# Kernel optimization log

Hardware: AMD Instinct MI355X
Metric: run time of the kernel (lower is better)

## Reference

```python
import jax, jax.numpy as jnp
import numpy as np

EMB = 1024
HEADS = 16
HEAD_DIM = EMB // HEADS


def setup_inputs() -> dict:
    key = jax.random.key(0)
    ks = jax.random.split(key, 9)
    s = 1.0 / np.sqrt(EMB)  # torch Linear default init scale (uniform), use normal*s for simplicity of magnitude
    x = jax.random.normal(ks[0], (2, 2048, EMB), dtype=jnp.float32)
    wQ = jax.random.uniform(ks[1], (EMB, EMB), jnp.float32, -s, s)
    bQ = jax.random.uniform(ks[2], (EMB,), jnp.float32, -s, s)
    wK = jax.random.uniform(ks[3], (EMB, EMB), jnp.float32, -s, s)
    bK = jax.random.uniform(ks[4], (EMB,), jnp.float32, -s, s)
    wV = jax.random.uniform(ks[5], (EMB, EMB), jnp.float32, -s, s)
    bV = jax.random.uniform(ks[6], (EMB,), jnp.float32, -s, s)
    wO = jax.random.uniform(ks[7], (EMB, EMB), jnp.float32, -s, s)
    bO = jax.random.uniform(ks[8], (EMB,), jnp.float32, -s, s)
    return {"x": x, "wQ": wQ, "bQ": bQ, "wK": wK, "bK": bK, "wV": wV, "bV": bV, "wO": wO, "bO": bO}


def reference(x, wQ, bQ, wK, bK, wV, bV, wO, bO):
    B, S, E = x.shape
    H, Dh = HEADS, HEAD_DIM
    # manual LayerNorm-like scaling; torch.std uses unbiased (ddof=1)
    mu = jnp.mean(x, axis=-1, keepdims=True)
    sd = jnp.std(x, axis=-1, keepdims=True, ddof=1)
    xn = (x - mu) / (sd + 1e-6)
    # torch Linear: y = x @ W.T + b
    q = (xn @ wQ.T + bQ).reshape(B, S, H, Dh).transpose(0, 2, 1, 3)  # [B,H,S,Dh]
    k = (xn @ wK.T + bK).reshape(B, S, H, Dh).transpose(0, 2, 1, 3)
    v = (xn @ wV.T + bV).reshape(B, S, H, Dh).transpose(0, 2, 1, 3)
    scores = jnp.einsum('bhsd,bhtd->bhst', q, k) / np.sqrt(Dh).astype(np.float32)
    A = jax.nn.softmax(scores, axis=-1)
    Hout = jnp.einsum('bhst,bhtd->bhsd', A, v)  # [B,H,S,Dh]
    Hout = Hout.transpose(0, 2, 1, 3).reshape(B, S, E)
    return Hout @ wO.T + bO
```

## Files before the change

kernel.cpp:

```cpp
#include <hip/hip_runtime.h>
#include <cstdint>
#include <cstddef>

typedef __bf16 bf16x8 __attribute__((ext_vector_type(8)));
typedef float f32x4 __attribute__((ext_vector_type(4)));
typedef unsigned short us4 __attribute__((ext_vector_type(4)));
typedef unsigned short us8 __attribute__((ext_vector_type(8)));
typedef unsigned int ui4 __attribute__((ext_vector_type(4)));
typedef unsigned short u16;

#define QSCALE 0.18033688011112042f

#define MFMA16(a, b, c) __builtin_amdgcn_mfma_f32_16x16x32_bf16((a), (b), (c), 0, 0, 0)
#define GLOAD16(g, l)                                                        \
  __builtin_amdgcn_global_load_lds(                                          \
      (const __attribute__((address_space(1))) void*)(g),                    \
      (__attribute__((address_space(3))) void*)(l), 16, 0, 0)

__device__ __forceinline__ u16 f2bf(float x) {
  unsigned int u = __float_as_uint(x);
  unsigned int r = u + 0x7fffu + ((u >> 16) & 1u);
  return (u16)(r >> 16);
}

__global__ __launch_bounds__(256) void prep_kernel(
    const float* __restrict__ x, const float* __restrict__ wq,
    const float* __restrict__ wk, const float* __restrict__ wv,
    const float* __restrict__ wo, u16* __restrict__ xn,
    u16* __restrict__ wdst) {
  const int bid = blockIdx.x;
  const int t = threadIdx.x;
  if (bid < 4096) {
    const int row = bid;
    const float* xr = x + (size_t)row * 1024;
    float4 v = *(const float4*)(xr + t * 4);
    float s = v.x + v.y + v.z + v.w;
    float s2 = v.x * v.x + v.y * v.y + v.z * v.z + v.w * v.w;
#pragma unroll
    for (int o = 32; o >= 1; o >>= 1) {
      s += __shfl_xor(s, o);
      s2 += __shfl_xor(s2, o);
    }
    __shared__ float red[8];
    const int wv_ = t >> 6, ln = t & 63;
    if (ln == 0) {
      red[wv_] = s;
      red[4 + wv_] = s2;
    }
    __syncthreads();
    s = red[0] + red[1] + red[2] + red[3];
    s2 = red[4] + red[5] + red[6] + red[7];
    const float mu = s * (1.0f / 1024.0f);
    float var = (s2 - 1024.0f * mu * mu) * (1.0f / 1023.0f);
    var = fmaxf(var, 0.0f);
    const float inv = 1.0f / (sqrtf(var) + 1e-6f);
    us4 o;
    o.x = f2bf((v.x - mu) * inv);
    o.y = f2bf((v.y - mu) * inv);
    o.z = f2bf((v.z - mu) * inv);
    o.w = f2bf((v.w - mu) * inv);
    *(us4*)(xn + (size_t)row * 1024 + t * 4) = o;
  } else {
    const int wid = bid - 4096;
    const int mat = wid >> 9, xi = wid & 511;
    const float* src = (mat == 0) ? wq : (mat == 1) ? wk : (mat == 2) ? wv : wo;
    const float sc = (mat == 0) ? QSCALE : 1.0f;
    u16* d = wdst + ((size_t)mat << 20);
    const size_t i = ((size_t)xi * 256 + t) * 8;
    float4 a = *(const float4*)(src + i);
    float4 b = *(const float4*)(src + i + 4);
    us8 o;
    o[0] = f2bf(a.x * sc);
    o[1] = f2bf(a.y * sc);
    o[2] = f2bf(a.z * sc);
    o[3] = f2bf(a.w * sc);
    o[4] = f2bf(b.x * sc);
    o[5] = f2bf(b.y * sc);
    o[6] = f2bf(b.z * sc);
    o[7] = f2bf(b.w * sc);
    *(us8*)(d + i) = o;
  }
}

__device__ __forceinline__ void gemm128_core(const u16* __restrict__ A,
                                             const u16* __restrict__ W,
                                             int m0, int n0,
                                             u16 (*As)[128 * 32],
                                             u16 (*Bs)[128 * 32],
                                             f32x4 acc[4][4]) {
  const int tid = threadIdx.x;
  const int lane = tid & 63, wave = tid >> 6;
  const int wm = wave >> 1, wn = wave & 1;
  const int lr = lane & 15, lg = lane >> 4;

  auto stage = [&](int buf, int kt) {
#pragma unroll
    for (int i = 0; i < 2; i++) {
      const int idx = i * 256 + tid;
      const int row = idx >> 2, ch = idx & 3;
      const int sc = ch ^ ((row >> 1) & 3);
      GLOAD16(A + (size_t)(m0 + row) * 1024 + kt * 32 + sc * 8,
              &As[buf][idx * 8]);
      GLOAD16(W + (size_t)(n0 + row) * 1024 + kt * 32 + sc * 8,
              &Bs[buf][idx * 8]);
    }
  };

  stage(0, 0);
  const int cs = (lg ^ ((lr >> 1) & 3)) * 8;
  int cur = 0;
  for (int kt = 0; kt < 32; ++kt) {
    __syncthreads();
    if (kt + 1 < 32) stage(cur ^ 1, kt + 1);
    bf16x8 af[4], bfr[4];
#pragma unroll
    for (int m = 0; m < 4; m++)
      af[m] = *(const bf16x8*)&As[cur][(wm * 64 + m * 16 + lr) * 32 + cs];
#pragma unroll
    for (int n = 0; n < 4; n++)
      bfr[n] = *(const bf16x8*)&Bs[cur][(wn * 64 + n * 16 + lr) * 32 + cs];
#pragma unroll
    for (int m = 0; m < 4; m++)
#pragma unroll
      for (int n = 0; n < 4; n++)
        acc[m][n] = MFMA16(af[m], bfr[n], acc[m][n]);
    cur ^= 1;
  }
}

__global__ __launch_bounds__(256) void qkv_gemm(
    const u16* __restrict__ xn, const u16* __restrict__ Wall,
    const float* __restrict__ bQ, const float* __restrict__ bK,
    const float* __restrict__ bV, u16* __restrict__ Qb, u16* __restrict__ Kb,
    u16* __restrict__ VTb) {
  __shared__ u16 As[2][128 * 32];
  __shared__ u16 Bs[2][128 * 32];
  const int z = blockIdx.z;
  const u16* W = Wall + ((size_t)z << 20);
  const float* bias = (z == 0) ? bQ : (z == 1) ? bK : bV;
  const float bscale = (z == 0) ? QSCALE : 1.0f;
  const int m0 = blockIdx.x * 128, n0 = blockIdx.y * 128;
  f32x4 acc[4][4] = {};
  gemm128_core(xn, W, m0, n0, As, Bs, acc);

  const int lane = threadIdx.x & 63, wave = threadIdx.x >> 6;
  const int wm = wave >> 1, wn = wave & 1, lr = lane & 15, lg = lane >> 4;
  if (z == 2) {
#pragma unroll
    for (int n = 0; n < 4; n++) {
      const int col = n0 + wn * 64 + n * 16 + lr;
      const float bv = bias[col];
      const int hh = col >> 6, d = col & 63;
#pragma unroll
      for (int m = 0; m < 4; m++) {
        const int rb = m0 + wm * 64 + m * 16 + lg * 4;
#pragma unroll
        for (int j = 0; j < 4; j++) {
          const int row = rb + j;
          const int bb = row >> 11, s = row & 2047;
          VTb[(((size_t)(bb * 16 + hh) * 64 + d) << 11) + s] =
              f2bf(acc[m][n][j] + bv);
        }
      }
    }
  } else {
    u16* o = (z == 0) ? Qb : Kb;
#pragma unroll
    for (int n = 0; n < 4; n++) {
      const int col = n0 + wn * 64 + n * 16 + lr;
      const float bv = bias[col] * bscale;
#pragma unroll
      for (int m = 0; m < 4; m++) {
        const int rb = m0 + wm * 64 + m * 16 + lg * 4;
#pragma unroll
        for (int j = 0; j < 4; j++)
          o[(size_t)(rb + j) * 1024 + col] = f2bf(acc[m][n][j] + bv);
      }
    }
  }
}

__global__ __launch_bounds__(256) void o_gemm(const u16* __restrict__ A,
                                              const u16* __restrict__ W,
                                              const float* __restrict__ bias,
                                              float* __restrict__ out) {
  __shared__ u16 As[2][128 * 32];
  __shared__ u16 Bs[2][128 * 32];
  const int m0 = blockIdx.x * 128, n0 = blockIdx.y * 128;
  f32x4 acc[4][4] = {};
  gemm128_core(A, W, m0, n0, As, Bs, acc);
  const int lane = threadIdx.x & 63, wave = threadIdx.x >> 6;
  const int wm = wave >> 1, wn = wave & 1, lr = lane & 15, lg = lane >> 4;
#pragma unroll
  for (int n = 0; n < 4; n++) {
    const int col = n0 + wn * 64 + n * 16 + lr;
    const float bv = bias[col];
#pragma unroll
    for (int m = 0; m < 4; m++) {
      const int rb = m0 + wm * 64 + m * 16 + lg * 4;
#pragma unroll
      for (int j = 0; j < 4; j++)
        out[(size_t)(rb + j) * 1024 + col] = acc[m][n][j] + bv;
    }
  }
}

__global__ __launch_bounds__(256, 2) void attn_kernel(
    const u16* __restrict__ Qb, const u16* __restrict__ Kb,
    const u16* __restrict__ VTb, u16* __restrict__ Hb) {
  __shared__ u16 Ks[2][128 * 64];
  __shared__ u16 Vs[2][64 * 128];
  const int tid = threadIdx.x;
  const int wave = tid >> 6, lane = tid & 63;
  const int lr = lane & 15, lg = lane >> 4;
  const int qb = blockIdx.x, bh = blockIdx.y;
  const int b = bh >> 4, h = bh & 15;

  bf16x8 aq[2][2];
#pragma unroll
  for (int qg = 0; qg < 2; qg++) {
    const int qrow = b * 2048 + qb * 128 + wave * 32 + qg * 16 + lr;
    const u16* qsrc = Qb + (size_t)qrow * 1024 + h * 64 + lg * 8;
    aq[qg][0] = *(const bf16x8*)qsrc;
    aq[qg][1] = *(const bf16x8*)(qsrc + 32);
  }

  float l_run[2] = {0.0f, 0.0f};
  f32x4 oacc[2][4] = {};

  auto stage = [&](int buf, int kt) {
#pragma unroll
    for (int i = 0; i < 4; i++) {
      const int idx = i * 256 + tid;
      const int r = idx >> 3, c = idx & 7;
      GLOAD16(Kb + (size_t)(b * 2048 + kt * 128 + r) * 1024 + h * 64 +
                  (c ^ (r & 7)) * 8,
              &Ks[buf][idx * 8]);
    }
#pragma unroll
    for (int i = 0; i < 4; i++) {
      const int idx = i * 256 + tid;
      const int r = idx >> 4, c = idx & 15;
      GLOAD16(VTb + (size_t)(bh * 64 + r) * 2048 + kt * 128 +
                  (c ^ (r & 7)) * 8,
              &Vs[buf][idx * 8]);
    }
  };

  auto softpack = [&](f32x4 (&s)[8], float& lsum, ui4 (&pf)[4]) {
    float ls = 0.0f;
#pragma unroll
    for (int n = 0; n < 8; n++) {
#pragma unroll
      for (int j = 0; j < 4; j++) {
        s[n][j] = __builtin_amdgcn_exp2f(s[n][j]);
        ls += s[n][j];
      }
    }
    lsum += ls;
    unsigned int w[8][2];
#pragma unroll
    for (int n = 0; n < 8; n++) {
      asm("v_cvt_pk_bf16_f32 %0, %1, %2"
          : "=v"(w[n][0])
          : "v"(s[n][0]), "v"(s[n][1]));
      asm("v_cvt_pk_bf16_f32 %0, %1, %2"
          : "=v"(w[n][1])
          : "v"(s[n][2]), "v"(s[n][3]));
    }
#pragma unroll
    for (int ks = 0; ks < 4; ks++) {
      unsigned int pw[4];
#pragma unroll
      for (int rp = 0; rp < 2; rp++) {
        unsigned int a = w[2 * ks][rp], bb = w[2 * ks + 1][rp];
        asm("v_permlane32_swap_b32 %0, %1" : "+v"(a), "+v"(bb));
        asm("v_permlane16_swap_b32 %0, %1" : "+v"(a), "+v"(bb));
        pw[rp] = a;
        pw[2 + rp] = bb;
      }
      pf[ks] = (ui4){pw[0], pw[1], pw[2], pw[3]};
    }
  };

  stage(0, 0);
  int cur = 0;
  for (int kt = 0; kt < 16; ++kt) {
    __syncthreads();
    if (kt + 1 < 16) stage(cur ^ 1, kt + 1);

    f32x4 s0[8], s1[8];
#pragma unroll
    for (int n = 0; n < 8; n++) {
      s0[n] = (f32x4){0.f, 0.f, 0.f, 0.f};
      s1[n] = (f32x4){0.f, 0.f, 0.f, 0.f};
    }
    __builtin_amdgcn_s_setprio(1);
#pragma unroll
    for (int n = 0; n < 8; n++) {
      const int row = n * 16 + lr;
#pragma unroll
      for (int ks = 0; ks < 2; ks++) {
        const int byo = (ks * 64 + lg * 16) ^ ((row & 7) << 4);
        const bf16x8 kfr = *(const bf16x8*)&Ks[cur][row * 64 + (byo >> 1)];
        s0[n] = MFMA16(kfr, aq[0][ks], s0[n]);
        s1[n] = MFMA16(kfr, aq[1][ks], s1[n]);
      }
    }
    __builtin_amdgcn_s_setprio(0);

    ui4 pf0[4], pf1[4];
    softpack(s0, l_run[0], pf0);
    softpack(s1, l_run[1], pf1);

    __builtin_amdgcn_s_setprio(1);
#pragma unroll
    for (int ks = 0; ks < 4; ks++) {
#pragma unroll
      for (int n = 0; n < 4; n++) {
        const int row = n * 16 + lr;
        const int byo = (ks * 64 + lg * 16) ^ ((row & 7) << 4);
        const bf16x8 vb = *(const bf16x8*)&Vs[cur][row * 128 + (byo >> 1)];
        oacc[0][n] = MFMA16(__builtin_bit_cast(bf16x8, pf0[ks]), vb, oacc[0][n]);
        oacc[1][n] = MFMA16(__builtin_bit_cast(bf16x8, pf1[ks]), vb, oacc[1][n]);
      }
    }
    __builtin_amdgcn_s_setprio(0);
    cur ^= 1;
  }

#pragma unroll
  for (int qg = 0; qg < 2; qg++) {
    float l = l_run[qg];
    l += __shfl_xor(l, 16);
    l += __shfl_xor(l, 32);
    float rl[4];
#pragma unroll
    for (int j = 0; j < 4; j++) rl[j] = 1.0f / __shfl(l, lg * 4 + j);
    const int hrow_base = b * 2048 + qb * 128 + wave * 32 + qg * 16 + lg * 4;
#pragma unroll
    for (int n = 0; n < 4; n++) {
      const int col = h * 64 + n * 16 + lr;
#pragma unroll
      for (int j = 0; j < 4; j++) {
        const float val = oacc[qg][n][j] * rl[j];
        Hb[(size_t)(hrow_base + j) * 1024 + col] = f2bf(val);
      }
    }
  }
}

extern "C" void kernel_launch(void* const* d_in, const int* in_sizes, int n_in,
                              void* d_out, int out_size, void* d_ws,
                              size_t ws_size, hipStream_t stream) {
  const float* x = (const float*)d_in[0];
  const float* wQ = (const float*)d_in[1];
  const float* bQ = (const float*)d_in[2];
  const float* wK = (const float*)d_in[3];
  const float* bK = (const float*)d_in[4];
  const float* wV = (const float*)d_in[5];
  const float* bV = (const float*)d_in[6];
  const float* wO = (const float*)d_in[7];
  const float* bO = (const float*)d_in[8];
  float* out = (float*)d_out;

  char* ws = (char*)d_ws;
  u16* xn = (u16*)(ws);
  u16* Wall = (u16*)(ws + ((size_t)8 << 20));
  u16* Qb = (u16*)(ws + ((size_t)16 << 20));
  u16* Kb = (u16*)(ws + ((size_t)24 << 20));
  u16* VTb = (u16*)(ws + ((size_t)32 << 20));
  u16* Hb = (u16*)(ws + ((size_t)40 << 20));

  prep_kernel<<<6144, 256, 0, stream>>>(x, wQ, wK, wV, wO, xn, Wall);
  qkv_gemm<<<dim3(32, 8, 3), 256, 0, stream>>>(xn, Wall, bQ, bK, bV, Qb, Kb,
                                               VTb);
  attn_kernel<<<dim3(16, 32), 256, 0, stream>>>(Qb, Kb, VTb, Hb);
  o_gemm<<<dim3(32, 8), 256, 0, stream>>>(Hb, Wall + ((size_t)3 << 20), bO,
                                          out);
}
```

Measured before the change: 132.4 us.

## Load GEMM fragments directly from global memory, dropping LDS staging

```diff
diff --git a/kernel.cpp b/kernel.cpp
--- a/kernel.cpp
+++ b/kernel.cpp
@@ -82,66 +82,45 @@
   }
 }
 
-__device__ __forceinline__ void gemm128_core(const u16* __restrict__ A,
-                                             const u16* __restrict__ W,
-                                             int m0, int n0,
-                                             u16 (*As)[128 * 32],
-                                             u16 (*Bs)[128 * 32],
-                                             f32x4 acc[4][4]) {
+__device__ __forceinline__ void gemm128_direct(const u16* __restrict__ A,
+                                               const u16* __restrict__ W,
+                                               int m0, int n0,
+                                               f32x4 acc[4][4]) {
   const int tid = threadIdx.x;
   const int lane = tid & 63, wave = tid >> 6;
   const int wm = wave >> 1, wn = wave & 1;
   const int lr = lane & 15, lg = lane >> 4;
-
-  auto stage = [&](int buf, int kt) {
-#pragma unroll
-    for (int i = 0; i < 2; i++) {
-      const int idx = i * 256 + tid;
-      const int row = idx >> 2, ch = idx & 3;
-      const int sc = ch ^ ((row >> 1) & 3);
-      GLOAD16(A + (size_t)(m0 + row) * 1024 + kt * 32 + sc * 8,
-              &As[buf][idx * 8]);
-      GLOAD16(W + (size_t)(n0 + row) * 1024 + kt * 32 + sc * 8,
-              &Bs[buf][idx * 8]);
-    }
-  };
-
-  stage(0, 0);
-  const int cs = (lg ^ ((lr >> 1) & 3)) * 8;
-  int cur = 0;
+  const u16* pa = A + (size_t)(m0 + wm * 64 + lr) * 1024 + lg * 8;
+  const u16* pw = W + (size_t)(n0 + wn * 64 + lr) * 1024 + lg * 8;
+#pragma unroll 4
   for (int kt = 0; kt < 32; ++kt) {
-    __syncthreads();
-    if (kt + 1 < 32) stage(cur ^ 1, kt + 1);
     bf16x8 af[4], bfr[4];
 #pragma unroll
     for (int m = 0; m < 4; m++)
-      af[m] = *(const bf16x8*)&As[cur][(wm * 64 + m * 16 + lr) * 32 + cs];
+      af[m] = *(const bf16x8*)(pa + (size_t)m * 16384 + kt * 32);
 #pragma unroll
     for (int n = 0; n < 4; n++)
-      bfr[n] = *(const bf16x8*)&Bs[cur][(wn * 64 + n * 16 + lr) * 32 + cs];
+      bfr[n] = *(const bf16x8*)(pw + (size_t)n * 16384 + kt * 32);
 #pragma unroll
     for (int m = 0; m < 4; m++)
 #pragma unroll
       for (int n = 0; n < 4; n++)
         acc[m][n] = MFMA16(af[m], bfr[n], acc[m][n]);
-    cur ^= 1;
-  }
-}
-
-__global__ __launch_bounds__(256) void qkv_gemm(
+  }
+}
+
+__global__ __launch_bounds__(256, 3) void qkv_gemm(
     const u16* __restrict__ xn, const u16* __restrict__ Wall,
     const float* __restrict__ bQ, const float* __restrict__ bK,
     const float* __restrict__ bV, u16* __restrict__ Qb, u16* __restrict__ Kb,
     u16* __restrict__ VTb) {
-  __shared__ u16 As[2][128 * 32];
-  __shared__ u16 Bs[2][128 * 32];
   const int z = blockIdx.z;
   const u16* W = Wall + ((size_t)z << 20);
   const float* bias = (z == 0) ? bQ : (z == 1) ? bK : bV;
   const float bscale = (z == 0) ? QSCALE : 1.0f;
   const int m0 = blockIdx.x * 128, n0 = blockIdx.y * 128;
   f32x4 acc[4][4] = {};
-  gemm128_core(xn, W, m0, n0, As, Bs, acc);
+  gemm128_direct(xn, W, m0, n0, acc);
 
   const int lane = threadIdx.x & 63, wave = threadIdx.x >> 6;
   const int wm = wave >> 1, wn = wave & 1, lr = lane & 15, lg = lane >> 4;
@@ -180,15 +159,13 @@
   }
 }
 
-__global__ __launch_bounds__(256) void o_gemm(const u16* __restrict__ A,
-                                              const u16* __restrict__ W,
-                                              const float* __restrict__ bias,
-                                              float* __restrict__ out) {
-  __shared__ u16 As[2][128 * 32];
-  __shared__ u16 Bs[2][128 * 32];
+__global__ __launch_bounds__(256, 3) void o_gemm(const u16* __restrict__ A,
+                                                 const u16* __restrict__ W,
+                                                 const float* __restrict__ bias,
+                                                 float* __restrict__ out) {
   const int m0 = blockIdx.x * 128, n0 = blockIdx.y * 128;
   f32x4 acc[4][4] = {};
-  gemm128_core(A, W, m0, n0, As, Bs, acc);
+  gemm128_direct(A, W, m0, n0, acc);
   const int lane = threadIdx.x & 63, wave = threadIdx.x >> 6;
   const int wm = wave >> 1, wn = wave & 1, lr = lane & 15, lg = lane >> 4;
 #pragma unroll
```

New measurement: 179.0 us. 1.35x slower.
